# Performance work log

Hardware: AMD Instinct MI355X
Metric: run time of the kernel (lower is better)

## Reference

```python
import jax, jax.numpy as jnp
import numpy as np

N = 86016      # 1024 graphs x 84 nodes
E = 4194304    # directed edges
H = 32         # hidden size
B = 1024       # graphs per batch
NPG = 84       # nodes per graph (hardcoded in original forward)
DEPTH = 4      # args.depth
NEG_SLOPE = 0.2


def setup_inputs() -> dict:
    key = jax.random.key(0)
    ks = jax.random.split(key, 12)
    s = 0.1
    return {
        "x": jax.random.normal(ks[0], (N, 1), jnp.float32),
        "edge_index": jax.random.randint(ks[1], (2, E), 0, N, jnp.int64 if jax.config.jax_enable_x64 else jnp.int32),
        "edge_attr": jax.random.normal(ks[2], (E, 2), jnp.float32),
        "W0": jax.random.normal(ks[3], (1, H), jnp.float32) * s,
        "Ws": jax.random.normal(ks[4], (DEPTH - 1, H, H), jnp.float32) * s,
        "att_src": jax.random.normal(ks[5], (DEPTH, H), jnp.float32) * s,
        "att_dst": jax.random.normal(ks[6], (DEPTH, H), jnp.float32) * s,
        "We": jax.random.normal(ks[7], (DEPTH, 2, H), jnp.float32) * s,
        "att_edge": jax.random.normal(ks[8], (DEPTH, H), jnp.float32) * s,
        "bias": jnp.zeros((DEPTH, H), jnp.float32),
        "lin_w": jax.random.normal(ks[9], (H, 1), jnp.float32) * s,
        "lin_b": jnp.zeros((1,), jnp.float32),
    }


def _gat_layer(h_in, src, dst, ea, W, a_s, a_d, We_l, a_e, b):
    """PyG GATConv, heads=1, edge_dim set, self-loops already appended.
    src/dst: [E+N] indices; ea: [E+N, edge_dim] edge attrs (with mean-filled loops)."""
    h = h_in @ W                                  # [N, H]
    alpha_src = h @ a_s                           # [N]
    alpha_dst = h @ a_d                           # [N]
    # fold lin_edge + att_edge: (ea @ We) @ a_e == ea @ (We @ a_e) -> avoids [E,H]
    alpha_edge = ea @ (We_l @ a_e)                # [E+N]
    logits = alpha_src[src] + alpha_dst[dst] + alpha_edge
    logits = jnp.where(logits >= 0, logits, NEG_SLOPE * logits)  # leaky_relu(0.2)
    # segment softmax over destination nodes (every node has a self-loop -> nonempty)
    m = jax.ops.segment_max(logits, dst, num_segments=N)
    w = jnp.exp(logits - m[dst])
    denom = jax.ops.segment_sum(w, dst, num_segments=N)
    alpha = w / denom[dst]                        # [E+N]
    out = jax.ops.segment_sum(alpha[:, None] * h[src], dst, num_segments=N)
    return out + b


def reference(x, edge_index, edge_attr, W0, Ws, att_src, att_dst, We, att_edge, bias, lin_w, lin_b):
    src0, dst0 = edge_index[0], edge_index[1]
    # add_self_loops with fill_value='mean': per-dst mean of incoming edge attrs
    deg = jax.ops.segment_sum(jnp.ones((E,), x.dtype), dst0, num_segments=N)
    ea_loop = jax.ops.segment_sum(edge_attr, dst0, num_segments=N) / jnp.maximum(deg, 1.0)[:, None]
    loops = jnp.arange(N, dtype=src0.dtype)
    src = jnp.concatenate([src0, loops])
    dst = jnp.concatenate([dst0, loops])
    ea = jnp.concatenate([edge_attr, ea_loop], axis=0)

    # layer 0 (+ relu; dropout is identity in eval)
    h = _gat_layer(x, src, dst, ea, W0, att_src[0], att_dst[0], We[0], att_edge[0], bias[0])
    h = jax.nn.relu(h)
    # middle layers
    for i in range(1, DEPTH - 1):
        h = _gat_layer(h, src, dst, ea, Ws[i - 1], att_src[i], att_dst[i], We[i], att_edge[i], bias[i])
        h = jax.nn.relu(h)
    # last layer: no relu/dropout
    h = _gat_layer(h, src, dst, ea, Ws[DEPTH - 2], att_src[DEPTH - 1], att_dst[DEPTH - 1],
                   We[DEPTH - 1], att_edge[DEPTH - 1], bias[DEPTH - 1])

    # global_add_pool over 84-node graphs, then linear + relu
    graph_ids = jnp.repeat(jnp.arange(B), NPG)    # [N]
    pooled = jax.ops.segment_sum(h, graph_ids, num_segments=B)  # [B, H]
    return jax.nn.relu(pooled @ lin_w + lin_b)    # [B, 1]
```

## Files before the change

kernel.cpp:

```cpp
#include <hip/hip_runtime.h>

#define N_NODES 86016
#define N_EDGES 4194304
#define HID 32
#define B_GR 1024
#define NPG 84
#define NEG 0.2f

#define NCH 512
#define CHE 8192
#define NB  512
#define NPB 168
#define SRCMASK 0x1FFFF

typedef float floatx2 __attribute__((ext_vector_type(2)));

constexpr size_t O_REC   = 0;
constexpr size_t O_CM    = O_REC  + (size_t)N_EDGES * 8;
constexpr size_t O_HT    = O_CM   + (size_t)NB * NCH * 4;
constexpr size_t O_HB    = O_HT   + (size_t)N_NODES * HID;
constexpr size_t O_AS    = O_HB   + (size_t)N_NODES * HID * 4;
constexpr size_t O_AD    = O_AS   + (size_t)N_NODES * 4;
constexpr size_t O_ROW   = O_AD   + (size_t)N_NODES * 4;
constexpr size_t O_BTOT  = O_ROW  + (size_t)(N_NODES + 1) * 4 + 12;
constexpr size_t O_BBASE = O_BTOT + (size_t)NB * 4;
constexpr size_t O_FOLD  = O_BBASE + (size_t)(NB + 1) * 4 + 12;

__device__ __forceinline__ unsigned short f2bf(float f) {
    unsigned u = __float_as_uint(f);
    u += 0x7FFFu + ((u >> 16) & 1u);
    return (unsigned short)(u >> 16);
}

__global__ __launch_bounds__(1024) void k_hist(const int* __restrict__ dst, int* __restrict__ cm) {
    __shared__ int cnt[NB];
    int t = threadIdx.x, c = blockIdx.x;
    if (t < NB) cnt[t] = 0;
    __syncthreads();
    int base = c * CHE;
#pragma unroll
    for (int k = 0; k < 8; ++k) {
        int d = dst[base + k * 1024 + t];
        atomicAdd(&cnt[(unsigned)d / NPB], 1);
    }
    __syncthreads();
    if (t < NB) cm[t * NCH + c] = cnt[t];
}

__global__ __launch_bounds__(512) void k_scanchunks(int* __restrict__ cm, int* __restrict__ btot) {
    __shared__ int sa[NCH], sb[NCH];
    int b = blockIdx.x, t = threadIdx.x;
    sa[t] = cm[b * NCH + t];
    __syncthreads();
    int* s = sa; int* d = sb;
    for (int off = 1; off < NCH; off <<= 1) {
        d[t] = s[t] + (t >= off ? s[t - off] : 0);
        __syncthreads();
        int* tmp = s; s = d; d = tmp;
    }
    cm[b * NCH + t] = t ? s[t - 1] : 0;
    if (t == 0) btot[b] = s[NCH - 1];
}

__global__ void k_scanbuckets(const int* __restrict__ btot, int* __restrict__ bbase,
                              int* __restrict__ row,
                              const float* __restrict__ We, const float* __restrict__ ae,
                              float* __restrict__ fold) {
    __shared__ int sa[NB], sb[NB];
    int t = threadIdx.x;
    if (t < 8) {
        int l = t >> 1, c = t & 1;
        float s = 0.f;
        for (int j = 0; j < 32; ++j) s += We[l * 64 + c * 32 + j] * ae[l * 32 + j];
        fold[t] = s;
    }
    sa[t] = btot[t];
    __syncthreads();
    int* s = sa; int* d = sb;
    for (int off = 1; off < NB; off <<= 1) {
        d[t] = s[t] + (t >= off ? s[t - off] : 0);
        __syncthreads();
        int* tmp = s; s = d; d = tmp;
    }
    bbase[t] = t ? s[t - 1] : 0;
    if (t == NB - 1) { bbase[NB] = s[NB - 1]; row[N_NODES] = s[NB - 1]; }
}

__global__ __launch_bounds__(1024) void k_place(const int* __restrict__ ei,
                                                const float2* __restrict__ ea,
                                                const int* __restrict__ cm,
                                                const int* __restrict__ bbase,
                                                int2* __restrict__ rec) {
    __shared__ int cnt[NB];
    __shared__ int base[NB];
    int t = threadIdx.x, c = blockIdx.x;
    if (t < NB) cnt[t] = 0;
    __syncthreads();
    int eb = c * CHE;
    int wd0[8], bin[8], rnk[8];
    unsigned pk[8];
#pragma unroll
    for (int k = 0; k < 8; ++k) {
        int e = eb + k * 1024 + t;
        int s = ei[e];
        int d = ei[N_EDGES + e];
        float2 a = ea[e];
        int b = (unsigned)d / NPB;
        int dn = d - b * NPB;
        wd0[k] = s | (dn << 17);
        pk[k] = ((unsigned)f2bf(a.y) << 16) | f2bf(a.x);
        bin[k] = b;
        rnk[k] = atomicAdd(&cnt[b], 1);
    }
    __syncthreads();
    if (t < NB) base[t] = bbase[t] + cm[t * NCH + c];
    __syncthreads();
#pragma unroll
    for (int k = 0; k < 8; ++k)
        rec[base[bin[k]] + rnk[k]] = make_int2(wd0[k], (int)pk[k]);
}

__global__ __launch_bounds__(1024) void k_sort(int2* __restrict__ rec,
                                               const int* __restrict__ bbase,
                                               int* __restrict__ row) {
    __shared__ int cnt[256], tmp[256], ebase[256];
    int b = blockIdx.x, t = threadIdx.x;
    int n0 = b * NPB;
    int beg = bbase[b], end = bbase[b + 1], m = end - beg;
    if (t < 256) cnt[t] = 0;
    __syncthreads();
    int2 rv[12];
    int dr[12];
    int cv = 0;
    for (int i = t; i < m; i += 1024) {
        int2 r = rec[beg + i];
        int dn = ((unsigned)r.x >> 17) & 0xFF;
        int rnk = atomicAdd(&cnt[dn], 1);
        if (cv < 12) { rv[cv] = r; dr[cv] = dn | (rnk << 8); }
        cv++;
    }
    __syncthreads();
    int* s = cnt; int* d = tmp;
    for (int off = 1; off < 256; off <<= 1) {
        int v = 0;
        if (t < 256) v = s[t] + (t >= off ? s[t - off] : 0);
        __syncthreads();
        if (t < 256) d[t] = v;
        __syncthreads();
        int* tp = s; s = d; d = tp;
    }
    if (t < 256) ebase[t] = t ? s[t - 1] : 0;
    __syncthreads();
    if (t < NPB) row[n0 + t] = beg + ebase[t];
    int ncv = cv < 12 ? cv : 12;
    for (int k = 0; k < ncv; ++k) {
        int dn = dr[k] & 0xFF;
        int rnk = dr[k] >> 8;
        rec[beg + ebase[dn] + rnk] = rv[k];
    }
}

__device__ __forceinline__ void store_fp8_pair(unsigned short* __restrict__ hout,
                                               int n, int j, float acc) {
    float p = __shfl_xor(acc, 1);
    if (!(j & 1)) {
        int pk = __builtin_amdgcn_cvt_pk_fp8_f32(acc, p, 0, false);
        hout[(n << 4) + (j >> 1)] = (unsigned short)pk;
    }
}

__global__ void k_transform0(const float* __restrict__ x, const float* __restrict__ W0,
                             const float* __restrict__ as_w, const float* __restrict__ ad_w,
                             unsigned short* __restrict__ hout, float* __restrict__ as_arr,
                             float* __restrict__ ad_arr) {
    int tid = blockIdx.x * 256 + threadIdx.x;
    int j = tid & 31;
    int n = tid >> 5;
    float acc = x[n] * W0[j];
    store_fp8_pair(hout, n, j, acc);
    float v1 = acc * as_w[j], v2 = acc * ad_w[j];
#pragma unroll
    for (int m = 16; m >= 1; m >>= 1) {
        v1 += __shfl_xor(v1, m);
        v2 += __shfl_xor(v2, m);
    }
    if (j == 0) { as_arr[n] = v1; ad_arr[n] = v2; }
}

__global__ void k_transform(const float* __restrict__ hin, const float* __restrict__ W,
                            const float* __restrict__ as_w, const float* __restrict__ ad_w,
                            unsigned short* __restrict__ hout, float* __restrict__ as_arr,
                            float* __restrict__ ad_arr) {
    __shared__ float Wl[1024];
    int t = threadIdx.x;
#pragma unroll
    for (int i = 0; i < 4; ++i) Wl[t + i * 256] = W[t + i * 256];
    __syncthreads();
    int tid = blockIdx.x * 256 + t;
    int j = tid & 31;
    int n = tid >> 5;
    float hv = hin[tid];
    float acc = 0.f;
#pragma unroll
    for (int k = 0; k < 32; ++k) acc += __shfl(hv, k, 32) * Wl[k * 32 + j];
    store_fp8_pair(hout, n, j, acc);
    float v1 = acc * as_w[j], v2 = acc * ad_w[j];
#pragma unroll
    for (int m = 16; m >= 1; m >>= 1) {
        v1 += __shfl_xor(v1, m);
        v2 += __shfl_xor(v2, m);
    }
    if (j == 0) { as_arr[n] = v1; ad_arr[n] = v2; }
}

__device__ __forceinline__ void acc4_fp8_pk(floatx2 w2, int word, floatx2* acc) {
    floatx2 v01 = __builtin_amdgcn_cvt_pk_f32_fp8(word, false);
    floatx2 v23 = __builtin_amdgcn_cvt_pk_f32_fp8(word, true);
    acc[0] = __builtin_elementwise_fma(w2, v01, acc[0]);
    acc[1] = __builtin_elementwise_fma(w2, v23, acc[1]);
}

__global__ void k_gather(const unsigned short* __restrict__ hT, const int2* __restrict__ rec,
                         const int* __restrict__ row,
                         const float* __restrict__ as_arr, const float* __restrict__ ad_arr,
                         const float* __restrict__ fold, const float* __restrict__ bias,
                         float* __restrict__ out, int do_relu) {
    const int2* hv = (const int2*)hT;
    int lane = threadIdx.x & 63;
    int n = blockIdx.x * 4 + (threadIdx.x >> 6);
    int slot = lane >> 2;
    int dl = lane & 3;
    int beg = row[n], end = row[n + 1];
    float c_dst = ad_arr[n];
    float f0 = fold[0], f1 = fold[1];
    floatx2 acc2[4];
    floatx2 zz = {0.f, 0.f};
    acc2[0] = zz; acc2[1] = zz; acc2[2] = zz; acc2[3] = zz;
    float den = 0.f, esum = 0.f;
    for (int e = beg; e < end; e += 64) {
        int ee = e + lane;
        bool act = ee < end;
        int2 r = rec[act ? ee : end - 1];
        int s = r.x & SRCMASK;
        float a = as_arr[s];
        float ax = __uint_as_float((unsigned)r.y << 16);
        float ay = __uint_as_float((unsigned)r.y & 0xFFFF0000u);
        float ed = fmaf(ax, f0, ay * f1);
        float lg = a + c_dst + ed;
        lg = fmaxf(lg, NEG * lg);
        float w = act ? __expf(lg) : 0.f;
        den += w;
        esum += act ? ed : 0.f;
#pragma unroll
        for (int p = 0; p < 4; ++p) {
            int sl = p * 16 + slot;
            int sp = __shfl(s, sl);
            float wp = __shfl(w, sl);
            int2 h = hv[(sp << 2) + dl];
            floatx2 w2 = {wp, wp};
            acc4_fp8_pk(w2, h.x, acc2);
            acc4_fp8_pk(w2, h.y, acc2 + 2);
        }
    }
    float* accf = (float*)acc2;
    den += __shfl_xor(den, 1);
    den += __shfl_xor(den, 2);
    esum += __shfl_xor(esum, 1);
    esum += __shfl_xor(esum, 2);
#pragma unroll
    for (int m = 4; m <= 32; m <<= 1) {
#pragma unroll
        for (int k = 0; k < 8; ++k) accf[k] += __shfl_xor(accf[k], m);
        den += __shfl_xor(den, m);
        esum += __shfl_xor(esum, m);
    }
    int dg = end - beg;
    float el = esum / fmaxf((float)dg, 1.0f);
    float lg = as_arr[n] + c_dst + el;
    lg = fmaxf(lg, NEG * lg);
    float w = __expf(lg);
    den += w;
    int2 hs = hv[(n << 2) + dl];
    floatx2 w2 = {w, w};
    acc4_fp8_pk(w2, hs.x, acc2);
    acc4_fp8_pk(w2, hs.y, acc2 + 2);
    float rden = 1.0f / den;
    float o[8];
#pragma unroll
    for (int k = 0; k < 8; ++k) {
        o[k] = accf[k] * rden + bias[8 * dl + k];
        if (do_relu) o[k] = fmaxf(o[k], 0.f);
    }
    if (slot == 0) {
        float4 v0 = {o[0], o[1], o[2], o[3]};
        float4 v1 = {o[4], o[5], o[6], o[7]};
        *(float4*)(out + (n << 5) + 8 * dl) = v0;
        *(float4*)(out + (n << 5) + 8 * dl + 4) = v1;
    }
}

__global__ void k_pool(const float* __restrict__ h, const float* __restrict__ lw,
                       const float* __restrict__ lb, float* __restrict__ out) {
    int lane = threadIdx.x & 63;
    int g = blockIdx.x * 4 + (threadIdx.x >> 6);
    int j = lane & 31;
    int half = lane >> 5;
    const float* base = h + (size_t)g * NPG * HID;
    float acc = 0.f;
    for (int i = half; i < NPG; i += 2) acc += base[i * HID + j];
    acc += __shfl_xor(acc, 32);
    float v = acc * lw[j];
#pragma unroll
    for (int m = 16; m >= 1; m >>= 1) v += __shfl_xor(v, m);
    if (lane == 0) out[g] = fmaxf(v + lb[0], 0.f);
}

extern "C" void kernel_launch(void* const* d_in, const int* in_sizes, int n_in,
                              void* d_out, int out_size, void* d_ws, size_t ws_size,
                              hipStream_t stream) {
    const float* x        = (const float*)d_in[0];
    const int*   ei       = (const int*)d_in[1];
    const float* eattr    = (const float*)d_in[2];
    const float* W0       = (const float*)d_in[3];
    const float* Ws       = (const float*)d_in[4];
    const float* att_src  = (const float*)d_in[5];
    const float* att_dst  = (const float*)d_in[6];
    const float* We       = (const float*)d_in[7];
    const float* att_edge = (const float*)d_in[8];
    const float* bias     = (const float*)d_in[9];
    const float* lin_w    = (const float*)d_in[10];
    const float* lin_b    = (const float*)d_in[11];
    float* out = (float*)d_out;

    char* w = (char*)d_ws;
    int2*           rec    = (int2*)(w + O_REC);
    int*            cm     = (int*)(w + O_CM);
    unsigned short* hT     = (unsigned short*)(w + O_HT);
    float*          hB     = (float*)(w + O_HB);
    float*          as_arr = (float*)(w + O_AS);
    float*          ad_arr = (float*)(w + O_AD);
    int*            row    = (int*)(w + O_ROW);
    int*            btot   = (int*)(w + O_BTOT);
    int*            bbase  = (int*)(w + O_BBASE);
    float*          fold   = (float*)(w + O_FOLD);

    k_hist<<<NCH, 1024, 0, stream>>>(ei + N_EDGES, cm);
    k_scanchunks<<<NB, 512, 0, stream>>>(cm, btot);
    k_scanbuckets<<<1, NB, 0, stream>>>(btot, bbase, row, We, att_edge, fold);
    k_place<<<NCH, 1024, 0, stream>>>(ei, (const float2*)eattr, cm, bbase, rec);
    k_sort<<<NB, 1024, 0, stream>>>(rec, bbase, row);

    k_transform0<<<N_NODES * HID / 256, 256, 0, stream>>>(x, W0, att_src, att_dst,
                                                          hT, as_arr, ad_arr);
    k_gather<<<N_NODES / 4, 256, 0, stream>>>(hT, rec, row, as_arr, ad_arr,
                                              fold, bias, hB, 1);
    for (int l = 1; l < 4; ++l) {
        k_transform<<<N_NODES * HID / 256, 256, 0, stream>>>(
            hB, Ws + (size_t)(l - 1) * HID * HID, att_src + l * HID, att_dst + l * HID,
            hT, as_arr, ad_arr);
        k_gather<<<N_NODES / 4, 256, 0, stream>>>(hT, rec, row, as_arr, ad_arr,
                                                  fold + 2 * l, bias + l * HID, hB,
                                                  (l < 3) ? 1 : 0);
    }

    k_pool<<<B_GR / 4, 256, 0, stream>>>(hB, lin_w, lin_b, out);
}
```

Baseline: 505.6 us.

## Process two destination nodes per wavefront with LDS edge exchange in gather

```diff
diff --git a/kernel.cpp b/kernel.cpp
--- a/kernel.cpp
+++ b/kernel.cpp
@@ -213,9 +213,10 @@
     if (j == 0) { as_arr[n] = v1; ad_arr[n] = v2; }
 }
 
-__device__ __forceinline__ void acc4_fp8_pk(floatx2 w2, int word, floatx2* acc) {
+__device__ __forceinline__ void acc_word(float wp, int word, floatx2* acc) {
     floatx2 v01 = __builtin_amdgcn_cvt_pk_f32_fp8(word, false);
     floatx2 v23 = __builtin_amdgcn_cvt_pk_f32_fp8(word, true);
+    floatx2 w2 = {wp, wp};
     acc[0] = __builtin_elementwise_fma(w2, v01, acc[0]);
     acc[1] = __builtin_elementwise_fma(w2, v23, acc[1]);
 }
@@ -225,77 +226,104 @@
                          const float* __restrict__ as_arr, const float* __restrict__ ad_arr,
                          const float* __restrict__ fold, const float* __restrict__ bias,
                          float* __restrict__ out, int do_relu) {
-    const int2* hv = (const int2*)hT;
+    const int* hw = (const int*)hT;
+    __shared__ int2 exch[4][2][64];
     int lane = threadIdx.x & 63;
-    int n = blockIdx.x * 4 + (threadIdx.x >> 6);
-    int slot = lane >> 2;
-    int dl = lane & 3;
-    int beg = row[n], end = row[n + 1];
-    float c_dst = ad_arr[n];
+    int wv = threadIdx.x >> 6;
+    int slot = lane >> 3;
+    int dl = lane & 7;
+    int n0 = blockIdx.x * 8 + wv * 2;
+    int n1 = n0 + 1;
+    int beg0 = row[n0], end0 = row[n0 + 1];
+    int beg1 = row[n1], end1 = row[n1 + 1];
+    float cd0 = ad_arr[n0], cd1 = ad_arr[n1];
     float f0 = fold[0], f1 = fold[1];
-    floatx2 acc2[4];
     floatx2 zz = {0.f, 0.f};
-    acc2[0] = zz; acc2[1] = zz; acc2[2] = zz; acc2[3] = zz;
-    float den = 0.f, esum = 0.f;
-    for (int e = beg; e < end; e += 64) {
-        int ee = e + lane;
-        bool act = ee < end;
-        int2 r = rec[act ? ee : end - 1];
-        int s = r.x & SRCMASK;
-        float a = as_arr[s];
-        float ax = __uint_as_float((unsigned)r.y << 16);
-        float ay = __uint_as_float((unsigned)r.y & 0xFFFF0000u);
-        float ed = fmaf(ax, f0, ay * f1);
-        float lg = a + c_dst + ed;
-        lg = fmaxf(lg, NEG * lg);
-        float w = act ? __expf(lg) : 0.f;
-        den += w;
-        esum += act ? ed : 0.f;
-#pragma unroll
-        for (int p = 0; p < 4; ++p) {
-            int sl = p * 16 + slot;
-            int sp = __shfl(s, sl);
-            float wp = __shfl(w, sl);
-            int2 h = hv[(sp << 2) + dl];
-            floatx2 w2 = {wp, wp};
-            acc4_fp8_pk(w2, h.x, acc2);
-            acc4_fp8_pk(w2, h.y, acc2 + 2);
+    floatx2 accA[2] = {zz, zz};
+    floatx2 accB[2] = {zz, zz};
+    float den0 = 0.f, esum0 = 0.f, den1 = 0.f, esum1 = 0.f;
+    for (int e0 = beg0, e1 = beg1; (e0 < end0) || (e1 < end1); e0 += 64, e1 += 64) {
+        int ee0 = e0 + lane, ee1 = e1 + lane;
+        int i0 = ee0 < end0 ? ee0 : end0 - 1; i0 = i0 < 0 ? 0 : i0;
+        int i1 = ee1 < end1 ? ee1 : end1 - 1; i1 = i1 < 0 ? 0 : i1;
+        int2 r0 = rec[i0];
+        int2 r1 = rec[i1];
+        int s0 = r0.x & SRCMASK;
+        int s1 = r1.x & SRCMASK;
+        float a0 = as_arr[s0];
+        float a1 = as_arr[s1];
+        float ax0 = __uint_as_float((unsigned)r0.y << 16);
+        float ay0 = __uint_as_float((unsigned)r0.y & 0xFFFF0000u);
+        float ax1 = __uint_as_float((unsigned)r1.y << 16);
+        float ay1 = __uint_as_float((unsigned)r1.y & 0xFFFF0000u);
+        float ed0 = fmaf(ax0, f0, ay0 * f1);
+        float ed1 = fmaf(ax1, f0, ay1 * f1);
+        float lg0 = a0 + cd0 + ed0;
+        float lg1 = a1 + cd1 + ed1;
+        lg0 = fmaxf(lg0, NEG * lg0);
+        lg1 = fmaxf(lg1, NEG * lg1);
+        bool act0 = ee0 < end0, act1 = ee1 < end1;
+        float w0 = act0 ? __expf(lg0) : 0.f;
+        float w1 = act1 ? __expf(lg1) : 0.f;
+        den0 += w0; den1 += w1;
+        esum0 += act0 ? ed0 : 0.f;
+        esum1 += act1 ? ed1 : 0.f;
+        exch[wv][0][lane] = make_int2(s0, __float_as_int(w0));
+        exch[wv][1][lane] = make_int2(s1, __float_as_int(w1));
+#pragma unroll
+        for (int p = 0; p < 8; ++p) {
+            int sl = p * 8 + slot;
+            int2 sw0 = exch[wv][0][sl];
+            int2 sw1 = exch[wv][1][sl];
+            int h0 = hw[(sw0.x << 3) + dl];
+            int h1 = hw[(sw1.x << 3) + dl];
+            acc_word(__int_as_float(sw0.y), h0, accA);
+            acc_word(__int_as_float(sw1.y), h1, accB);
         }
     }
-    float* accf = (float*)acc2;
-    den += __shfl_xor(den, 1);
-    den += __shfl_xor(den, 2);
-    esum += __shfl_xor(esum, 1);
-    esum += __shfl_xor(esum, 2);
-#pragma unroll
-    for (int m = 4; m <= 32; m <<= 1) {
-#pragma unroll
-        for (int k = 0; k < 8; ++k) accf[k] += __shfl_xor(accf[k], m);
-        den += __shfl_xor(den, m);
-        esum += __shfl_xor(esum, m);
-    }
-    int dg = end - beg;
-    float el = esum / fmaxf((float)dg, 1.0f);
-    float lg = as_arr[n] + c_dst + el;
-    lg = fmaxf(lg, NEG * lg);
-    float w = __expf(lg);
-    den += w;
-    int2 hs = hv[(n << 2) + dl];
-    floatx2 w2 = {w, w};
-    acc4_fp8_pk(w2, hs.x, acc2);
-    acc4_fp8_pk(w2, hs.y, acc2 + 2);
-    float rden = 1.0f / den;
-    float o[8];
-#pragma unroll
-    for (int k = 0; k < 8; ++k) {
-        o[k] = accf[k] * rden + bias[8 * dl + k];
-        if (do_relu) o[k] = fmaxf(o[k], 0.f);
+    float* fA = (float*)accA;
+    float* fB = (float*)accB;
+#pragma unroll
+    for (int m = 8; m <= 32; m <<= 1) {
+#pragma unroll
+        for (int k = 0; k < 4; ++k) {
+            fA[k] += __shfl_xor(fA[k], m);
+            fB[k] += __shfl_xor(fB[k], m);
+        }
+    }
+#pragma unroll
+    for (int m = 1; m <= 32; m <<= 1) {
+        den0 += __shfl_xor(den0, m);
+        den1 += __shfl_xor(den1, m);
+        esum0 += __shfl_xor(esum0, m);
+        esum1 += __shfl_xor(esum1, m);
+    }
+    int dg0 = end0 - beg0, dg1 = end1 - beg1;
+    float el0 = esum0 / fmaxf((float)dg0, 1.0f);
+    float el1 = esum1 / fmaxf((float)dg1, 1.0f);
+    float lgs0 = as_arr[n0] + cd0 + el0;
+    float lgs1 = as_arr[n1] + cd1 + el1;
+    lgs0 = fmaxf(lgs0, NEG * lgs0);
+    lgs1 = fmaxf(lgs1, NEG * lgs1);
+    float ws0 = __expf(lgs0), ws1 = __expf(lgs1);
+    den0 += ws0; den1 += ws1;
+    int hs0 = hw[(n0 << 3) + dl];
+    int hs1 = hw[(n1 << 3) + dl];
+    acc_word(ws0, hs0, accA);
+    acc_word(ws1, hs1, accB);
+    float rd0 = 1.0f / den0, rd1 = 1.0f / den1;
+    float4 bi = *(const float4*)(bias + 4 * dl);
+    float4 o0 = {fA[0] * rd0 + bi.x, fA[1] * rd0 + bi.y, fA[2] * rd0 + bi.z, fA[3] * rd0 + bi.w};
+    float4 o1 = {fB[0] * rd1 + bi.x, fB[1] * rd1 + bi.y, fB[2] * rd1 + bi.z, fB[3] * rd1 + bi.w};
+    if (do_relu) {
+        o0.x = fmaxf(o0.x, 0.f); o0.y = fmaxf(o0.y, 0.f);
+        o0.z = fmaxf(o0.z, 0.f); o0.w = fmaxf(o0.w, 0.f);
+        o1.x = fmaxf(o1.x, 0.f); o1.y = fmaxf(o1.y, 0.f);
+        o1.z = fmaxf(o1.z, 0.f); o1.w = fmaxf(o1.w, 0.f);
     }
     if (slot == 0) {
-        float4 v0 = {o[0], o[1], o[2], o[3]};
-        float4 v1 = {o[4], o[5], o[6], o[7]};
-        *(float4*)(out + (n << 5) + 8 * dl) = v0;
-        *(float4*)(out + (n << 5) + 8 * dl + 4) = v1;
+        *(float4*)(out + (n0 << 5) + (dl << 2)) = o0;
+        *(float4*)(out + (n1 << 5) + (dl << 2)) = o1;
     }
 }
 
@@ -352,13 +380,13 @@
 
     k_transform0<<<N_NODES * HID / 256, 256, 0, stream>>>(x, W0, att_src, att_dst,
                                                           hT, as_arr, ad_arr);
-    k_gather<<<N_NODES / 4, 256, 0, stream>>>(hT, rec, row, as_arr, ad_arr,
+    k_gather<<<N_NODES / 8, 256, 0, stream>>>(hT, rec, row, as_arr, ad_arr,
                                               fold, bias, hB, 1);
     for (int l = 1; l < 4; ++l) {
         k_transform<<<N_NODES * HID / 256, 256, 0, stream>>>(
             hB, Ws + (size_t)(l - 1) * HID * HID, att_src + l * HID, att_dst + l * HID,
             hT, as_arr, ad_arr);
-        k_gather<<<N_NODES / 4, 256, 0, stream>>>(hT, rec, row, as_arr, ad_arr,
+        k_gather<<<N_NODES / 8, 256, 0, stream>>>(hT, rec, row, as_arr, ad_arr,
                                                   fold + 2 * l, bias + l * HID, hB,
                                                   (l < 3) ? 1 : 0);
     }
```

New measurement: 481.1 us. -4.8%, faster.
